# Kernel tuning notes

Hardware: AMD Instinct MI355X
Metric: run time of the kernel (lower is better)

## Reference

```python
import jax, jax.numpy as jnp
import numpy as np
from jax import lax

B, C, H, W = 4, 64, 128, 128
G, K, CO = 8, 3, 64
KK = K * K
MC = G * KK  # mask channels = 72


def _conv3x3(x, w, b):
    # standard 3x3 conv, stride 1, padding 1, NCHW
    y = lax.conv_general_dilated(x, w, (1, 1), ((1, 1), (1, 1)),
                                 dimension_numbers=('NCHW', 'OIHW', 'NCHW'))
    return y + b[None, :, None, None]


def _deform_conv2d(x, offset, mask, w, b):
    """Modulated deformable conv (DCNv2), stride=1, padding=1, dilation=1.
    offset: [B, 2*G*KK, H, W] interpreted as [B, G, KK, 2(dy,dx), H, W] (torchvision layout).
    mask:   [B, G*KK, H, W].
    w: [Co, C/G, K, K], b: [Co].
    """
    Bn, Cn, Hn, Wn = x.shape
    Co, Cg, Kh, Kw = w.shape
    Gn = Cn // Cg
    KKn = Kh * Kw
    Ho, Wo = Hn, Wn  # stride 1, pad 1, k 3

    off = offset.reshape(Bn, Gn, KKn, 2, Ho, Wo)
    dy, dx = off[:, :, :, 0], off[:, :, :, 1]
    m = mask.reshape(Bn, Gn, 1, KKn, Ho, Wo)

    kh = (jnp.arange(KKn) // Kw).astype(x.dtype)  # kernel row index
    kw = (jnp.arange(KKn) % Kw).astype(x.dtype)
    hh = jnp.arange(Ho, dtype=x.dtype)
    ww = jnp.arange(Wo, dtype=x.dtype)
    # sampling positions: h - pad + kh*dil + dy  -> [B,G,KK,Ho,Wo]
    py = hh[None, None, None, :, None] - 1.0 + kh[None, None, :, None, None] + dy
    px = ww[None, None, None, None, :] - 1.0 + kw[None, None, :, None, None] + dx

    y0 = jnp.floor(py); x0 = jnp.floor(px)
    ly = py - y0; lx = px - x0
    y0i = y0.astype(jnp.int32); x0i = x0.astype(jnp.int32)
    y1i = y0i + 1; x1i = x0i + 1

    xg = x.reshape(Bn, Gn, Cg, Hn * Wn)

    def corner(yi, xi, wgt):
        valid = ((yi >= 0) & (yi < Hn) & (xi >= 0) & (xi < Wn)).astype(x.dtype)
        idx = (jnp.clip(yi, 0, Hn - 1) * Wn + jnp.clip(xi, 0, Wn - 1))
        idx = idx.reshape(Bn, Gn, 1, KKn * Ho * Wo)
        v = jnp.take_along_axis(xg, idx, axis=3).reshape(Bn, Gn, Cg, KKn, Ho, Wo)
        return v * (wgt * valid)[:, :, None]

    val = (corner(y0i, x0i, (1.0 - ly) * (1.0 - lx))
           + corner(y0i, x1i, (1.0 - ly) * lx)
           + corner(y1i, x0i, ly * (1.0 - lx))
           + corner(y1i, x1i, ly * lx))
    val = val * m  # modulation

    wr = w.reshape(Gn, Co // Gn, Cg, KKn)
    out = jnp.einsum('bgckhw,gock->bgohw', val, wr).reshape(Bn, Co, Ho, Wo)
    return out + b[None, :, None, None]


def setup_inputs() -> dict:
    key = jax.random.key(0)
    ks = jax.random.split(key, 8)
    f = lambda k, s, sc=1.0: jax.random.normal(k, s, dtype=jnp.float32) * sc
    return {
        'x': f(ks[0], (B, C, H, W)),
        'share_with_feat': f(ks[1], (B, C, H, W)),
        'offset_feat': f(ks[2], (B, C, H, W)),
        # conv_offset_mask: C -> 3*G*KK (zero-init in original; small random here)
        'w_om': f(ks[3], (3 * MC, C, 3, 3), 0.02),
        'b_om': jnp.zeros((3 * MC,), jnp.float32),
        'w_em1': f(ks[4], (C, 2 * C, 3, 3), 0.05),
        'b_em1': jnp.zeros((C,), jnp.float32),
        'w_em2': f(ks[5], (MC, C, 3, 3), 0.05),
        'b_em2': jnp.zeros((MC,), jnp.float32),
        # deform conv weight: [Co, C/G, 3, 3]
        'w_dc': f(ks[6], (CO, C // G, 3, 3), 0.05),
        'b_dc': f(ks[7], (CO,), 0.05),
    }


def reference(x, share_with_feat, offset_feat, w_om, b_om, w_em1, b_em1,
              w_em2, b_em2, w_dc, b_dc):
    om = _conv3x3(offset_feat, w_om, b_om)
    o1, o2, mask_x = jnp.split(om, 3, axis=1)
    offset = jnp.concatenate([o1, o2], axis=1)
    mask_x = jax.nn.sigmoid(mask_x)
    x_deform = _deform_conv2d(x, offset, mask_x, w_dc, b_dc)
    # extra_mask=True branch
    em = _conv3x3(jnp.concatenate([share_with_feat, offset_feat], axis=1), w_em1, b_em1)
    em = jnp.where(em >= 0, em, 0.1 * em)  # LeakyReLU(0.1)
    em = jax.nn.sigmoid(_conv3x3(em, w_em2, b_em2))
    share_deform = _deform_conv2d(share_with_feat, offset, em, w_dc, b_dc)
    return (x_deform, share_deform)
```

## Files before the change

### kernel.cpp

```cpp
#include <hip/hip_runtime.h>
#include <math.h>

#define BB 4
#define CC 64
#define HH 128
#define WW 128
#define GG 8
#define COO 64
#define HWC (HH*WW)

#define DPAD 12
#define DROW 26

typedef float f32x16 __attribute__((ext_vector_type(16)));
typedef __bf16 bf16x8 __attribute__((ext_vector_type(8)));

__device__ __forceinline__ unsigned short bf16_rn(float f) {
    unsigned int u = __float_as_uint(f);
    unsigned int r = (u + 0x7fffu + ((u >> 16) & 1u)) >> 16;
    return (unsigned short)r;
}
__device__ __forceinline__ float b2f(unsigned short u) {
    return __uint_as_float(((unsigned int)u) << 16);
}

__global__ __launch_bounds__(256) void pack_inputs_kernel(
    const float* __restrict__ x, const float* __restrict__ share,
    const float* __restrict__ offf,
    unsigned int* __restrict__ xs, unsigned short* __restrict__ sc16,
    unsigned short* __restrict__ oc16)
{
    __shared__ unsigned short lds[64][66];
    const int b = blockIdx.y;
    const int pix0 = blockIdx.x * 64;
    const int t = threadIdx.x;
    const int p = t & 63, q = t >> 6;
    const int pl = t & 63, cg = t >> 6;

#pragma unroll
    for (int i = 0; i < 16; i++) {
        int c = i * 4 + q;
        size_t idx = ((size_t)b * 64 + c) * HWC + pix0 + p;
        unsigned short sb = bf16_rn(share[idx]);
        lds[c][p] = sb;
        xs[idx] = (unsigned int)bf16_rn(x[idx]) | ((unsigned int)sb << 16);
    }
    __syncthreads();
    {
        unsigned int u[8];
#pragma unroll
        for (int j = 0; j < 8; j++) {
            unsigned int lo = lds[cg * 16 + 2 * j][pl];
            unsigned int hi = lds[cg * 16 + 2 * j + 1][pl];
            u[j] = lo | (hi << 16);
        }
        unsigned int* dst = (unsigned int*)(sc16 + ((size_t)(b * 4 + cg) * HWC + pix0 + pl) * 16);
        *(uint4*)dst = make_uint4(u[0], u[1], u[2], u[3]);
        *(uint4*)(dst + 4) = make_uint4(u[4], u[5], u[6], u[7]);
    }
    __syncthreads();

#pragma unroll
    for (int i = 0; i < 16; i++) {
        int c = i * 4 + q;
        lds[c][p] = bf16_rn(offf[((size_t)b * 64 + c) * HWC + pix0 + p]);
    }
    __syncthreads();
    {
        unsigned int u[8];
#pragma unroll
        for (int j = 0; j < 8; j++) {
            unsigned int lo = lds[cg * 16 + 2 * j][pl];
            unsigned int hi = lds[cg * 16 + 2 * j + 1][pl];
            u[j] = lo | (hi << 16);
        }
        unsigned int* dst = (unsigned int*)(oc16 + ((size_t)(b * 4 + cg) * HWC + pix0 + pl) * 16);
        *(uint4*)dst = make_uint4(u[0], u[1], u[2], u[3]);
        *(uint4*)(dst + 4) = make_uint4(u[4], u[5], u[6], u[7]);
    }
}

__device__ __forceinline__ void pack_w_one(const float* __restrict__ w,
                                           unsigned short* __restrict__ wp,
                                           int Cout, int COP, int CinTot, int idx) {
    int i  = idx & 15;
    int co = (idx >> 4) % COP;
    int t  = idx / (16 * COP);
    int cg = t & 3;
    int kk = (t >> 2) % 9;
    int seg = t / 36;
    int cin = seg * 64 + cg * 16 + i;
    float v = (co < Cout) ? w[((size_t)co * CinTot + cin) * 9 + kk] : 0.f;
    wp[idx] = bf16_rn(v);
}

__global__ void pack_w_all_kernel(const float* __restrict__ w_om, unsigned short* __restrict__ wp_om,
                                  const float* __restrict__ w_em1, unsigned short* __restrict__ wp_em1,
                                  const float* __restrict__ w_em2, unsigned short* __restrict__ wp_em2) {
    int i = blockIdx.x * 256 + threadIdx.x;
    if (i < 147456) {
        pack_w_one(w_om, wp_om, 216, 256, 64, i);
    } else if (i < 147456 + 73728) {
        pack_w_one(w_em1, wp_em1, 64, 64, 128, i - 147456);
    } else if (i < 147456 + 73728 + 73728) {
        pack_w_one(w_em2, wp_em2, 72, 128, 64, i - 147456 - 73728);
    }
}

template<int NSEG, int MREP, int COP>
__global__ __launch_bounds__(256) void conv_mfma_kernel(
    const unsigned short* __restrict__ in0,
    const unsigned short* __restrict__ in1,
    const unsigned short* __restrict__ wp,
    const float* __restrict__ bias,
    void* __restrict__ out,
    int Cout, int out_mode, int act)
{
    constexpr int NT  = 2;
    constexpr int PXW = NT * 32 + 2;
    constexpr int NE  = 4 * 6 * PXW;
    __shared__ __align__(16) unsigned short slds[NE * 16];

    const int lane = threadIdx.x & 63;
    const int wid  = threadIdx.x >> 6;
    const int l31  = lane & 31;
    const int half = lane >> 5;
    int tmp = blockIdx.x;
    const int xsp = tmp & 1; tmp >>= 1;
    const int rb  = tmp & 31;
    const int b   = tmp >> 5;
    const int r0  = rb * 4;
    const int r   = r0 + wid;
    const int px0 = xsp * 64;
    const int co0 = blockIdx.y * (32 * MREP);

    f32x16 acc[MREP][NT];
#pragma unroll
    for (int m = 0; m < MREP; m++)
#pragma unroll
        for (int nt = 0; nt < NT; nt++)
#pragma unroll
            for (int rg = 0; rg < 16; rg++) acc[m][nt][rg] = 0.f;

    const int lbase = (wid * PXW + l31) * 16 + half * 8;

    for (int seg = 0; seg < NSEG; seg++) {
        const unsigned short* inb = (seg ? in1 : in0) + (size_t)b * 4 * HWC * 16;
        if (seg) __syncthreads();

        for (int e = threadIdx.x; e < NE; e += 256) {
            const int cg  = e / (6 * PXW);
            const int rem = e - cg * (6 * PXW);
            const int row = rem / PXW;
            const int px  = rem - row * PXW;
            const int iy = r0 - 1 + row;
            const int ix = px0 - 1 + px;
            const bool valid = ((unsigned)iy < (unsigned)HH) && ((unsigned)ix < (unsigned)WW);
            const int iyc = min(max(iy, 0), HH - 1);
            const int ixc = min(max(ix, 0), WW - 1);
            const uint4* src = (const uint4*)(inb + ((size_t)cg * HWC + (size_t)iyc * WW + ixc) * 16);
            uint4 v0, v1;
            if (valid) { v0 = src[0]; v1 = src[1]; }
            else       { v0 = make_uint4(0u, 0u, 0u, 0u); v1 = v0; }
            uint4* dst = (uint4*)(slds + (size_t)e * 16);
            dst[0] = v0; dst[1] = v1;
        }
        __syncthreads();

#pragma unroll
        for (int kk = 0; kk < 9; kk++) {
            const int kh = kk / 3, kw = kk % 3;
#pragma unroll
            for (int cg = 0; cg < 4; cg++) {
                const int t = (seg * 9 + kk) * 4 + cg;
                bf16x8 af[MREP];
#pragma unroll
                for (int m = 0; m < MREP; m++)
                    af[m] = *(const bf16x8*)(wp +
                        (size_t)(t * COP + co0 + m * 32 + l31) * 16 + half * 8);
#pragma unroll
                for (int nt = 0; nt < NT; nt++) {
                    const bf16x8 bf = *(const bf16x8*)(slds + lbase +
                        ((cg * 6 + kh) * PXW + nt * 32 + kw) * 16);
#pragma unroll
                    for (int m = 0; m < MREP; m++)
                        acc[m][nt] = __builtin_amdgcn_mfma_f32_32x32x16_bf16(
                            af[m], bf, acc[m][nt], 0, 0, 0);
                }
            }
        }
    }

#pragma unroll
    for (int m = 0; m < MREP; m++) {
#pragma unroll
        for (int nt = 0; nt < NT; nt++) {
#pragma unroll
            for (int rg = 0; rg < 16; rg++) {
                const int row = (rg & 3) + 8 * (rg >> 2) + 4 * half;
                const int co = co0 + m * 32 + row;
                if (co < Cout) {
                    float v = acc[m][nt][rg] + bias[co];
                    if (act == 1)      v = (v >= 0.f) ? v : 0.1f * v;
                    else if (act == 2) v = 1.f / (1.f + __expf(-v));
                    else if (act == 3 && co >= 144) v = 1.f / (1.f + __expf(-v));
                    const int pix = r * WW + px0 + nt * 32 + l31;
                    if (out_mode == 2)
                        ((unsigned short*)out)[((size_t)b * Cout + co) * HWC + pix] = bf16_rn(v);
                    else
                        ((unsigned short*)out)[((size_t)(b * 4 + (co >> 4)) * HWC + pix) * 16 + (co & 15)] = bf16_rn(v);
                }
            }
        }
    }
}

__global__ __launch_bounds__(256) void deform_fused_kernel(
    const unsigned int* __restrict__ xs,
    const unsigned short* __restrict__ om, const unsigned short* __restrict__ em,
    const float* __restrict__ wdc, const float* __restrict__ bdc,
    float* __restrict__ outx, float* __restrict__ outs)
{
    __shared__ __align__(16) unsigned int lds[24 * DROW * DPAD];

    const int bg = blockIdx.x >> 6;
    const int b = bg >> 3, g = bg & 7;
    const int tile = blockIdx.x & 63;
    const int r0 = (tile >> 3) << 4;
    const int c0 = (tile & 7) << 4;
    const int tx = threadIdx.x & 15, ty = threadIdx.x >> 4;
    const int h = r0 + ty, w = c0 + tx;
    const int wr0 = r0 - 4, wc0 = c0 - 4;

    const unsigned int* xsb = xs + ((size_t)b * 64 + g * 8) * HWC;

#pragma unroll
    for (int i = 0; i < 18; i++) {
        unsigned int slot = (unsigned int)threadIdx.x + i * 256u;
        unsigned int sx = slot % 24u;
        unsigned int t2 = slot / 24u;
        unsigned int sy = t2 % 24u;
        unsigned int c  = t2 / 24u;
        int iy = min(max(wr0 + (int)sy, 0), HH - 1);
        int ix = min(max(wc0 + (int)sx, 0), WW - 1);
        lds[(sy * DROW + sx) * DPAD + c] = xsb[(size_t)c * HWC + iy * WW + ix];
    }

    __syncthreads();

    const int pix = h * WW + w;
    const unsigned short* omb = om + (size_t)b * 216 * HWC + pix + (size_t)g * 18 * HWC;
    const unsigned short* mmb = om + (size_t)b * 216 * HWC + pix + (size_t)(144 + g * 9) * HWC;
    const unsigned short* emb = em + (size_t)b * 72 * HWC + pix + (size_t)g * 9 * HWC;

    float accx[8], accs[8];
#pragma unroll
    for (int o = 0; o < 8; o++) { accx[o] = 0.f; accs[o] = 0.f; }

#pragma unroll
    for (int kk = 0; kk < 9; kk++) {
        const float dy = b2f(omb[(size_t)(kk * 2) * HWC]);
        const float dx = b2f(omb[(size_t)(kk * 2 + 1) * HWC]);
        const float m1 = b2f(mmb[(size_t)kk * HWC]);
        const float m2 = b2f(emb[(size_t)kk * HWC]);

        const float py = (float)(h - 1 + kk / 3) + dy;
        const float px = (float)(w - 1 + kk % 3) + dx;
        const float y0f = floorf(py), x0f = floorf(px);
        const float ly = py - y0f, lx = px - x0f;
        const int y0 = (int)y0f, x0 = (int)x0f;
        const int y1 = y0 + 1, x1 = x0 + 1;
        const bool vy0 = (y0 >= 0) && (y0 < HH), vy1 = (y1 >= 0) && (y1 < HH);
        const bool vx0 = (x0 >= 0) && (x0 < WW), vx1 = (x1 >= 0) && (x1 < WW);
        float w00 = (1.f - ly) * (1.f - lx); if (!(vy0 && vx0)) w00 = 0.f;
        float w01 = (1.f - ly) * lx;         if (!(vy0 && vx1)) w01 = 0.f;
        float w10 = ly * (1.f - lx);         if (!(vy1 && vx0)) w10 = 0.f;
        float w11 = ly * lx;                 if (!(vy1 && vx1)) w11 = 0.f;
        const int cy0 = min(max(y0, 0), HH - 1), cy1 = min(max(y1, 0), HH - 1);
        const int cx0 = min(max(x0, 0), WW - 1), cx1 = min(max(x1, 0), WW - 1);

        const int sy0 = cy0 - wr0, sy1 = cy1 - wr0;
        const int sx0 = cx0 - wc0, sx1 = cx1 - wc0;
        const bool inw = (sy0 >= 0) && (sy1 < 24) && (sx0 >= 0) && (sx1 < 24);

        const float* wk = wdc + (size_t)g * 8 * 8 * 9 + kk;

        if (__builtin_expect(inw, 1)) {
            const int p00 = (sy0 * DROW + sx0) * DPAD, p01 = (sy0 * DROW + sx1) * DPAD;
            const int p10 = (sy1 * DROW + sx0) * DPAD, p11 = (sy1 * DROW + sx1) * DPAD;
#pragma unroll
            for (int ch = 0; ch < 2; ch++) {
                uint4 qa = *(const uint4*)(lds + p00 + ch * 4);
                uint4 qb = *(const uint4*)(lds + p01 + ch * 4);
                uint4 qc = *(const uint4*)(lds + p10 + ch * 4);
                uint4 qd = *(const uint4*)(lds + p11 + ch * 4);
                const unsigned int ua[4] = {qa.x, qa.y, qa.z, qa.w};
                const unsigned int ub[4] = {qb.x, qb.y, qb.z, qb.w};
                const unsigned int uc[4] = {qc.x, qc.y, qc.z, qc.w};
                const unsigned int ud[4] = {qd.x, qd.y, qd.z, qd.w};
#pragma unroll
                for (int j = 0; j < 4; j++) {
                    const int c = ch * 4 + j;
                    float x00 = __uint_as_float(ua[j] << 16), s00 = __uint_as_float(ua[j] & 0xffff0000u);
                    float x01 = __uint_as_float(ub[j] << 16), s01 = __uint_as_float(ub[j] & 0xffff0000u);
                    float x10 = __uint_as_float(uc[j] << 16), s10 = __uint_as_float(uc[j] & 0xffff0000u);
                    float x11 = __uint_as_float(ud[j] << 16), s11 = __uint_as_float(ud[j] & 0xffff0000u);
                    float vx = w00 * x00; vx = fmaf(w01, x01, vx); vx = fmaf(w10, x10, vx); vx = fmaf(w11, x11, vx);
                    float vs = w00 * s00; vs = fmaf(w01, s01, vs); vs = fmaf(w10, s10, vs); vs = fmaf(w11, s11, vs);
                    vx *= m1;
                    vs *= m2;
#pragma unroll
                    for (int o = 0; o < 8; o++) {
                        const float wv = wk[(size_t)(o * 8 + c) * 9];
                        accx[o] = fmaf(vx, wv, accx[o]);
                        accs[o] = fmaf(vs, wv, accs[o]);
                    }
                }
            }
        } else {
            const int i00 = cy0 * WW + cx0, i01 = cy0 * WW + cx1;
            const int i10 = cy1 * WW + cx0, i11 = cy1 * WW + cx1;
#pragma unroll
            for (int c = 0; c < 8; c++) {
                const unsigned int* xc = xsb + (size_t)c * HWC;
                unsigned int a = xc[i00], bq = xc[i01], cq = xc[i10], dq = xc[i11];
                float x00 = __uint_as_float(a << 16),  s00 = __uint_as_float(a & 0xffff0000u);
                float x01 = __uint_as_float(bq << 16), s01 = __uint_as_float(bq & 0xffff0000u);
                float x10 = __uint_as_float(cq << 16), s10 = __uint_as_float(cq & 0xffff0000u);
                float x11 = __uint_as_float(dq << 16), s11 = __uint_as_float(dq & 0xffff0000u);
                float vx = w00 * x00; vx = fmaf(w01, x01, vx); vx = fmaf(w10, x10, vx); vx = fmaf(w11, x11, vx);
                float vs = w00 * s00; vs = fmaf(w01, s01, vs); vs = fmaf(w10, s10, vs); vs = fmaf(w11, s11, vs);
                vx *= m1;
                vs *= m2;
#pragma unroll
                for (int o = 0; o < 8; o++) {
                    const float wv = wk[(size_t)(o * 8 + c) * 9];
                    accx[o] = fmaf(vx, wv, accx[o]);
                    accs[o] = fmaf(vs, wv, accs[o]);
                }
            }
        }
    }

#pragma unroll
    for (int o = 0; o < 8; o++) {
        const float bv = bdc[g * 8 + o];
        outx[((size_t)(b * COO + g * 8 + o)) * HWC + pix] = accx[o] + bv;
        outs[((size_t)(b * COO + g * 8 + o)) * HWC + pix] = accs[o] + bv;
    }
}

extern "C" void kernel_launch(void* const* d_in, const int* in_sizes, int n_in,
                              void* d_out, int out_size, void* d_ws, size_t ws_size,
                              hipStream_t stream) {
    const float* x      = (const float*)d_in[0];
    const float* share  = (const float*)d_in[1];
    const float* offf   = (const float*)d_in[2];
    const float* w_om   = (const float*)d_in[3];
    const float* b_om   = (const float*)d_in[4];
    const float* w_em1  = (const float*)d_in[5];
    const float* b_em1  = (const float*)d_in[6];
    const float* w_em2  = (const float*)d_in[7];
    const float* b_em2  = (const float*)d_in[8];
    const float* w_dc   = (const float*)d_in[9];
    const float* b_dc   = (const float*)d_in[10];

    unsigned int* xs = (unsigned int*)d_ws;
    unsigned short* us = (unsigned short*)(xs + 4194304);
    unsigned short* sc16   = us;
    unsigned short* oc16   = sc16 + 4194304;
    unsigned short* emm    = oc16 + 4194304;
    unsigned short* om_b   = emm + 4194304;
    unsigned short* em_b   = om_b + 14155776;
    unsigned short* wp_om  = em_b + 4718592;
    unsigned short* wp_em1 = wp_om + 147456;
    unsigned short* wp_em2 = wp_em1 + 73728;

    float* outx = (float*)d_out;
    float* outs = outx + 4194304;

    dim3 blk(256);

    pack_inputs_kernel<<<dim3(HWC / 64, BB), blk, 0, stream>>>(x, share, offf, xs, sc16, oc16);
    pack_w_all_kernel<<<(147456 + 73728 + 73728) / 256, blk, 0, stream>>>(
        w_om, wp_om, w_em1, wp_em1, w_em2, wp_em2);

    conv_mfma_kernel<1, 2, 256><<<dim3(256, 4), blk, 0, stream>>>(
        oc16, nullptr, wp_om, b_om, om_b, 216, 2, 3);
    conv_mfma_kernel<2, 1, 64><<<dim3(256, 2), blk, 0, stream>>>(
        sc16, oc16, wp_em1, b_em1, emm, 64, 3, 1);
    conv_mfma_kernel<1, 2, 128><<<dim3(256, 2), blk, 0, stream>>>(
        emm, nullptr, wp_em2, b_em2, em_b, 72, 2, 2);

    deform_fused_kernel<<<dim3(BB * GG * 64), blk, 0, stream>>>(
        xs, om_b, em_b, w_dc, b_dc, outx, outs);
}
```

Before: 296.9 us.

## Switch conv MFMA from 32x32x16 to 16x16x32 tiles with lane-packed weights

Rewrites the implicit-GEMM conv kernel to use 16x16x32 bf16 MFMA with a 4x4 grid of output-channel by pixel tiles per wave. The weights are repacked into a per-lane layout so each A fragment is a single contiguous 16-byte load. The LDS staging loop is fully unrolled. The em1 conv now runs 64 channels per block with half the grid in y. This aims to improve operand reuse and issue efficiency, at the cost of more LDS reads per MFMA and different register pressure.

After: 502.7 us. 69.3% more time.

```diff
diff --git a/kernel.cpp b/kernel.cpp
--- a/kernel.cpp
+++ b/kernel.cpp
@@ -12,7 +12,7 @@
 #define DPAD 12
 #define DROW 26
 
-typedef float f32x16 __attribute__((ext_vector_type(16)));
+typedef float f32x4 __attribute__((ext_vector_type(4)));
 typedef __bf16 bf16x8 __attribute__((ext_vector_type(8)));
 
 __device__ __forceinline__ unsigned short bf16_rn(float f) {
@@ -83,13 +83,21 @@
 __device__ __forceinline__ void pack_w_one(const float* __restrict__ w,
                                            unsigned short* __restrict__ wp,
                                            int Cout, int COP, int CinTot, int idx) {
-    int i  = idx & 15;
-    int co = (idx >> 4) % COP;
-    int t  = idx / (16 * COP);
-    int cg = t & 3;
-    int kk = (t >> 2) % 9;
-    int seg = t / 36;
-    int cin = seg * 64 + cg * 16 + i;
+    int j    = idx & 7;
+    int lane = (idx >> 3) & 63;
+    int rem  = idx >> 9;
+    int ncob = COP >> 4;
+    int cob  = rem % ncob;
+    int t    = rem / ncob;
+    int seg  = t / 18;
+    int tt   = t % 18;
+    int kk   = tt >> 1;
+    int ks   = tt & 1;
+    int co   = cob * 16 + (lane & 15);
+    int kl   = ((lane >> 4) << 3) + j;
+    int cg   = ks * 2 + (kl >> 4);
+    int ci   = kl & 15;
+    int cin  = seg * 64 + cg * 16 + ci;
     float v = (co < Cout) ? w[((size_t)co * CinTot + cin) * 9 + kk] : 0.f;
     wp[idx] = bf16_rn(v);
 }
@@ -107,7 +115,7 @@
     }
 }
 
-template<int NSEG, int MREP, int COP>
+template<int NSEG, int COP>
 __global__ __launch_bounds__(256) void conv_mfma_kernel(
     const unsigned short* __restrict__ in0,
     const unsigned short* __restrict__ in1,
@@ -116,15 +124,12 @@
     void* __restrict__ out,
     int Cout, int out_mode, int act)
 {
-    constexpr int NT  = 2;
-    constexpr int PXW = NT * 32 + 2;
+    constexpr int PXW = 66;
     constexpr int NE  = 4 * 6 * PXW;
     __shared__ __align__(16) unsigned short slds[NE * 16];
 
     const int lane = threadIdx.x & 63;
     const int wid  = threadIdx.x >> 6;
-    const int l31  = lane & 31;
-    const int half = lane >> 5;
     int tmp = blockIdx.x;
     const int xsp = tmp & 1; tmp >>= 1;
     const int rb  = tmp & 31;
@@ -132,38 +137,49 @@
     const int r0  = rb * 4;
     const int r   = r0 + wid;
     const int px0 = xsp * 64;
-    const int co0 = blockIdx.y * (32 * MREP);
-
-    f32x16 acc[MREP][NT];
-#pragma unroll
-    for (int m = 0; m < MREP; m++)
-#pragma unroll
-        for (int nt = 0; nt < NT; nt++)
-#pragma unroll
-            for (int rg = 0; rg < 16; rg++) acc[m][nt][rg] = 0.f;
-
-    const int lbase = (wid * PXW + l31) * 16 + half * 8;
-
+    const int cb0 = blockIdx.y * 4;
+    const int co0 = blockIdx.y * 64;
+
+    f32x4 acc[4][4];
+#pragma unroll
+    for (int cob = 0; cob < 4; cob++)
+#pragma unroll
+        for (int nt = 0; nt < 4; nt++)
+#pragma unroll
+            for (int rg = 0; rg < 4; rg++) acc[cob][nt][rg] = 0.f;
+
+    const int pxl  = lane & 15;
+    const int kgrp = lane >> 4;
+    const int cglh = lane >> 5;
+    const int cil0 = (kgrp & 1) * 8;
+    const unsigned short* lp = slds +
+        ((size_t)(cglh * 6 + wid) * PXW + 1 + pxl) * 16 + cil0;
+
+#pragma unroll
     for (int seg = 0; seg < NSEG; seg++) {
         const unsigned short* inb = (seg ? in1 : in0) + (size_t)b * 4 * HWC * 16;
         if (seg) __syncthreads();
 
-        for (int e = threadIdx.x; e < NE; e += 256) {
-            const int cg  = e / (6 * PXW);
-            const int rem = e - cg * (6 * PXW);
-            const int row = rem / PXW;
-            const int px  = rem - row * PXW;
-            const int iy = r0 - 1 + row;
-            const int ix = px0 - 1 + px;
-            const bool valid = ((unsigned)iy < (unsigned)HH) && ((unsigned)ix < (unsigned)WW);
-            const int iyc = min(max(iy, 0), HH - 1);
-            const int ixc = min(max(ix, 0), WW - 1);
-            const uint4* src = (const uint4*)(inb + ((size_t)cg * HWC + (size_t)iyc * WW + ixc) * 16);
-            uint4 v0, v1;
-            if (valid) { v0 = src[0]; v1 = src[1]; }
-            else       { v0 = make_uint4(0u, 0u, 0u, 0u); v1 = v0; }
-            uint4* dst = (uint4*)(slds + (size_t)e * 16);
-            dst[0] = v0; dst[1] = v1;
+#pragma unroll
+        for (int i = 0; i < 7; i++) {
+            const int e = (int)threadIdx.x + i * 256;
+            if (i < 6 || e < NE) {
+                const int cg  = e / (6 * PXW);
+                const int rem = e - cg * (6 * PXW);
+                const int row = rem / PXW;
+                const int px  = rem - row * PXW;
+                const int iy = r0 - 1 + row;
+                const int ix = px0 - 1 + px;
+                const bool valid = ((unsigned)iy < (unsigned)HH) && ((unsigned)ix < (unsigned)WW);
+                const int iyc = min(max(iy, 0), HH - 1);
+                const int ixc = min(max(ix, 0), WW - 1);
+                const uint4* src = (const uint4*)(inb + ((size_t)cg * HWC + (size_t)iyc * WW + ixc) * 16);
+                uint4 v0, v1;
+                if (valid) { v0 = src[0]; v1 = src[1]; }
+                else       { v0 = make_uint4(0u, 0u, 0u, 0u); v1 = v0; }
+                uint4* dst = (uint4*)(slds + (size_t)e * 16);
+                dst[0] = v0; dst[1] = v1;
+            }
         }
         __syncthreads();
 
@@ -171,40 +187,41 @@
         for (int kk = 0; kk < 9; kk++) {
             const int kh = kk / 3, kw = kk % 3;
 #pragma unroll
-            for (int cg = 0; cg < 4; cg++) {
-                const int t = (seg * 9 + kk) * 4 + cg;
-                bf16x8 af[MREP];
-#pragma unroll
-                for (int m = 0; m < MREP; m++)
-                    af[m] = *(const bf16x8*)(wp +
-                        (size_t)(t * COP + co0 + m * 32 + l31) * 16 + half * 8);
-#pragma unroll
-                for (int nt = 0; nt < NT; nt++) {
-                    const bf16x8 bf = *(const bf16x8*)(slds + lbase +
-                        ((cg * 6 + kh) * PXW + nt * 32 + kw) * 16);
-#pragma unroll
-                    for (int m = 0; m < MREP; m++)
-                        acc[m][nt] = __builtin_amdgcn_mfma_f32_32x32x16_bf16(
-                            af[m], bf, acc[m][nt], 0, 0, 0);
-                }
+            for (int ks = 0; ks < 2; ks++) {
+                const int t = seg * 18 + kk * 2 + ks;
+                bf16x8 af[4];
+#pragma unroll
+                for (int cob = 0; cob < 4; cob++)
+                    af[cob] = *(const bf16x8*)(wp +
+                        ((size_t)(t * (COP >> 4) + cb0 + cob) * 64 + lane) * 8);
+                bf16x8 bf[4];
+#pragma unroll
+                for (int nt = 0; nt < 4; nt++)
+                    bf[nt] = *(const bf16x8*)(lp +
+                        ((ks * 12 + kh) * PXW + nt * 16 + kw - 1) * 16);
+#pragma unroll
+                for (int cob = 0; cob < 4; cob++)
+#pragma unroll
+                    for (int nt = 0; nt < 4; nt++)
+                        acc[cob][nt] = __builtin_amdgcn_mfma_f32_16x16x32_bf16(
+                            af[cob], bf[nt], acc[cob][nt], 0, 0, 0);
             }
         }
     }
 
 #pragma unroll
-    for (int m = 0; m < MREP; m++) {
-#pragma unroll
-        for (int nt = 0; nt < NT; nt++) {
-#pragma unroll
-            for (int rg = 0; rg < 16; rg++) {
-                const int row = (rg & 3) + 8 * (rg >> 2) + 4 * half;
-                const int co = co0 + m * 32 + row;
+    for (int cob = 0; cob < 4; cob++) {
+#pragma unroll
+        for (int nt = 0; nt < 4; nt++) {
+#pragma unroll
+            for (int rg = 0; rg < 4; rg++) {
+                const int co = co0 + cob * 16 + kgrp * 4 + rg;
                 if (co < Cout) {
-                    float v = acc[m][nt][rg] + bias[co];
+                    float v = acc[cob][nt][rg] + bias[co];
                     if (act == 1)      v = (v >= 0.f) ? v : 0.1f * v;
                     else if (act == 2) v = 1.f / (1.f + __expf(-v));
                     else if (act == 3 && co >= 144) v = 1.f / (1.f + __expf(-v));
-                    const int pix = r * WW + px0 + nt * 32 + l31;
+                    const int pix = r * WW + px0 + nt * 16 + pxl;
                     if (out_mode == 2)
                         ((unsigned short*)out)[((size_t)b * Cout + co) * HWC + pix] = bf16_rn(v);
                     else
@@ -385,11 +402,11 @@
     pack_w_all_kernel<<<(147456 + 73728 + 73728) / 256, blk, 0, stream>>>(
         w_om, wp_om, w_em1, wp_em1, w_em2, wp_em2);
 
-    conv_mfma_kernel<1, 2, 256><<<dim3(256, 4), blk, 0, stream>>>(
+    conv_mfma_kernel<1, 256><<<dim3(256, 4), blk, 0, stream>>>(
         oc16, nullptr, wp_om, b_om, om_b, 216, 2, 3);
-    conv_mfma_kernel<2, 1, 64><<<dim3(256, 2), blk, 0, stream>>>(
+    conv_mfma_kernel<2, 64><<<dim3(256, 1), blk, 0, stream>>>(
         sc16, oc16, wp_em1, b_em1, emm, 64, 3, 1);
-    conv_mfma_kernel<1, 2, 128><<<dim3(256, 2), blk, 0, stream>>>(
+    conv_mfma_kernel<1, 128><<<dim3(256, 2), blk, 0, stream>>>(
         emm, nullptr, wp_em2, b_em2, em_b, 72, 2, 2);
 
     deform_fused_kernel<<<dim3(BB * GG * 64), blk, 0, stream>>>(
```
